# Kernel optimization log

Hardware: AMD Instinct MI355X
Metric: run time of the kernel (lower is better)

## Reference

```python
import jax, jax.numpy as jnp
import numpy as np

N = 100000      # num nodes (centers == sources here)
AVG_DEG = 16    # average degree -> ~1.6M edges
D_IN = 256
D_OUT = 128


def setup_inputs() -> dict:
    rng = np.random.default_rng(0)
    # random per-row degrees (some zeros allowed; gcn_norm masks inf -> 0)
    deg = rng.integers(0, 2 * AVG_DEG + 1, size=N)
    ptr = np.concatenate([[0], np.cumsum(deg)]).astype(np.int64)  # CSR row pointers [N+1]
    E = int(ptr[-1])
    idx = rng.integers(0, N, size=E).astype(np.int64)             # source node per edge
    dst = np.repeat(np.arange(N, dtype=np.int64), deg)            # destination node per edge

    key = jax.random.key(0)
    k1, k2 = jax.random.split(key)
    x = jax.random.normal(k1, (N, D_IN), dtype=jnp.float32)
    # glorot-ish init for Linear weight [out, in] (bias=False)
    W = jax.random.normal(k2, (D_OUT, D_IN), dtype=jnp.float32) * (1.0 / np.sqrt(D_IN))
    return {
        "x": x,
        "W": W,
        "ptr": jnp.asarray(ptr),
        "idx": jnp.asarray(idx),
        "dst": jnp.asarray(dst),
    }


def reference(x, W, ptr, idx, dst):
    # mm_before: in_channels (256) > out_channels (128) -> linear first
    h = x @ W.T  # [N, D_OUT]
    # gcn_norm: per-edge value = 1/deg(dst), inf -> 0
    deg = (ptr[1:] - ptr[:-1]).astype(jnp.float32)            # [N]
    inv_deg = jnp.where(deg > 0, 1.0 / jnp.maximum(deg, 1.0), 0.0)
    edge_value = inv_deg[dst]                                  # [E]
    # CSR weighted neighbor aggregation (SpMM): out[i] = sum_e ev[e] * h[idx[e]]
    msgs = h[idx] * edge_value[:, None]                        # [E, D_OUT]
    out = jax.ops.segment_sum(msgs, dst, num_segments=N)      # [N, D_OUT]
    return out
```

## Files before the change

### kernel.cpp

```cpp
#include <hip/hip_runtime.h>
#include <hip/hip_bf16.h>

typedef __attribute__((ext_vector_type(4))) float f32x4;
typedef __attribute__((ext_vector_type(8))) short s16x8;
typedef __attribute__((ext_vector_type(4))) short s16x4;
typedef __attribute__((ext_vector_type(4))) unsigned int u32x4;
typedef __attribute__((ext_vector_type(2))) unsigned int u32x2;

#define NODES 100000
#define SROW (NODES + 1)
#define DIN 256
#define DOUT 128
#define NSLICE 2
#define SLICE_CH 64

static __device__ inline unsigned short f2bf(float f) {
    __hip_bfloat16 h = __float2bfloat16(f);
    return __builtin_bit_cast(unsigned short, h);
}
static __device__ inline float lo2f(unsigned int v) {
    return __builtin_bit_cast(float, v << 16);
}
static __device__ inline float hi2f(unsigned int v) {
    return __builtin_bit_cast(float, v & 0xffff0000u);
}

__global__ __launch_bounds__(256) void gcn_prep(const float* __restrict__ W,
                                                const int* __restrict__ ptr,
                                                unsigned short* __restrict__ wsW,
                                                float* __restrict__ inv_deg,
                                                unsigned short* __restrict__ h_s) {
    int t = blockIdx.x * 256 + threadIdx.x;
    if (t < DOUT * DIN) wsW[t] = f2bf(W[t]);
    if (t < NODES) {
        int d = ptr[t + 1] - ptr[t];
        inv_deg[t] = d > 0 ? 1.0f / (float)d : 0.0f;
    }
    if (t < NSLICE * SLICE_CH)
        h_s[(long)(t >> 6) * ((long)SROW * SLICE_CH) + (long)NODES * SLICE_CH + (t & 63)] = 0;
}

__global__ __launch_bounds__(256) void gcn_gemm(const float* __restrict__ x,
                                                const unsigned short* __restrict__ wsW,
                                                unsigned short* __restrict__ h_s) {
    const int tid  = threadIdx.x;
    const int lane = tid & 63;
    const int wid  = tid >> 6;
    const int row0 = blockIdx.x * 128;
    const int lr = lane & 15;
    const int lg = lane >> 4;

    __shared__ unsigned short ldsA[128 * 64];
    __shared__ unsigned short ldsB[128 * 64];

    const int st_sub = tid >> 4;
    const int st_c4  = (tid & 15) * 4;

    f32x4 ar[8];
    u32x2 br[8];

#define LOADA(C) { _Pragma("unroll") for (int j = 0; j < 8; ++j) { \
        int grow = row0 + j * 16 + st_sub; \
        grow = grow < NODES ? grow : NODES - 1;  \
        ar[j] = *reinterpret_cast<const f32x4*>(x + (long)grow * DIN + (C) * 64 + st_c4); } }

#define LOADB(C) { _Pragma("unroll") for (int j = 0; j < 8; ++j) { \
        const int out = j * 16 + st_sub; \
        br[j] = *reinterpret_cast<const u32x2*>(wsW + out * DIN + (C) * 64 + st_c4); } }

#define STAGE() { _Pragma("unroll") for (int j = 0; j < 8; ++j) { \
        const int row = j * 16 + st_sub; \
        const int idx = row * 64 + (st_c4 ^ ((row & 7) << 3)); \
        s16x4 pa; \
        pa[0] = (short)f2bf(ar[j][0]); pa[1] = (short)f2bf(ar[j][1]); \
        pa[2] = (short)f2bf(ar[j][2]); pa[3] = (short)f2bf(ar[j][3]); \
        *reinterpret_cast<s16x4*>(ldsA + idx) = pa; \
        *reinterpret_cast<u32x2*>(ldsB + idx) = br[j]; } }

#define COMPUTE() { _Pragma("unroll") for (int ks = 0; ks < 2; ++ks) { \
        s16x8 a[2], b[8]; \
        _Pragma("unroll") for (int m = 0; m < 2; ++m) { \
            const int row = wid * 32 + m * 16 + lr; \
            const int idx = row * 64 + ((ks * 32 + lg * 8) ^ ((row & 7) << 3)); \
            a[m] = *reinterpret_cast<const s16x8*>(ldsA + idx); } \
        _Pragma("unroll") for (int n = 0; n < 8; ++n) { \
            const int out = n * 16 + lr; \
            const int idx = out * 64 + ((ks * 32 + lg * 8) ^ ((out & 7) << 3)); \
            b[n] = *reinterpret_cast<const s16x8*>(ldsB + idx); } \
        _Pragma("unroll") for (int n = 0; n < 8; ++n) { \
            acc[0][n] = __builtin_amdgcn_mfma_f32_16x16x32_bf16(a[0], b[n], acc[0][n], 0, 0, 0); \
            acc[1][n] = __builtin_amdgcn_mfma_f32_16x16x32_bf16(a[1], b[n], acc[1][n], 0, 0, 0); } } }

    f32x4 acc[2][8];
#pragma unroll
    for (int m = 0; m < 2; ++m)
#pragma unroll
        for (int n = 0; n < 8; ++n) acc[m][n] = (f32x4)(0.0f);

    LOADA(0); LOADB(0);
    STAGE();
    __syncthreads();
    LOADA(1); LOADB(1);
    COMPUTE();
    __syncthreads();
    STAGE();
    __syncthreads();
    LOADA(2); LOADB(2);
    COMPUTE();
    __syncthreads();
    STAGE();
    __syncthreads();
    LOADA(3); LOADB(3);
    COMPUTE();
    __syncthreads();
    STAGE();
    __syncthreads();
    COMPUTE();

#pragma unroll
    for (int m = 0; m < 2; ++m) {
        const int rbase = row0 + wid * 32 + m * 16 + lg * 4;
#pragma unroll
        for (int n = 0; n < 8; ++n) {
            const long sb = (long)(n >> 2) * ((long)SROW * SLICE_CH);
            const int ch = (n & 3) * 16 + lr;
#pragma unroll
            for (int r = 0; r < 4; ++r) {
                const int row = rbase + r;
                if (row < NODES)
                    h_s[sb + (long)row * SLICE_CH + ch] = f2bf(acc[m][n][r]);
            }
        }
    }
#undef LOADA
#undef LOADB
#undef STAGE
#undef COMPUTE
}

__global__ __launch_bounds__(320) void gcn_agg(const int* __restrict__ ptr,
                                               const int* __restrict__ idx,
                                               const unsigned short* __restrict__ h_s,
                                               const float* __restrict__ inv_deg,
                                               float* __restrict__ out, int E) {
    const int lane  = threadIdx.x & 63;
    const int wid   = threadIdx.x >> 6;
    const int q     = blockIdx.x & 7;
    const int slice = q >> 2;
    const int chunk = (blockIdx.x >> 3) * 4 + (q & 3);
    const int g     = lane >> 3;
    const int c     = lane & 7;
    const int node  = chunk * 40 + wid * 8 + g;

    const int p0  = ptr[node];
    const int deg = ptr[node + 1] - p0;
    const int Em1 = E - 1;
    const float w = inv_deg[node];

    int r[4];
#pragma unroll
    for (int j = 0; j < 4; ++j) {
        int a = p0 + c + 8 * j;
        a = a < Em1 ? a : Em1;
        r[j] = idx[a];
    }

    const unsigned short* hb = h_s + (long)slice * ((long)SROW * SLICE_CH) + c * 8;

    float acc[8];
#pragma unroll
    for (int t = 0; t < 8; ++t) acc[t] = 0.0f;

#pragma unroll
    for (int e = 0; e < 32; ++e) {
        int s = __shfl(r[e >> 3], (lane & 56) | (e & 7));
        s = e < deg ? s : NODES;
        const u32x4 v = *reinterpret_cast<const u32x4*>(hb + (long)s * SLICE_CH);
        acc[0] += lo2f(v[0]); acc[1] += hi2f(v[0]);
        acc[2] += lo2f(v[1]); acc[3] += hi2f(v[1]);
        acc[4] += lo2f(v[2]); acc[5] += hi2f(v[2]);
        acc[6] += lo2f(v[3]); acc[7] += hi2f(v[3]);
    }

    float* op = out + (long)node * DOUT + slice * SLICE_CH + c * 8;
    f32x4 o0, o1;
    o0[0] = acc[0] * w; o0[1] = acc[1] * w; o0[2] = acc[2] * w; o0[3] = acc[3] * w;
    o1[0] = acc[4] * w; o1[1] = acc[5] * w; o1[2] = acc[6] * w; o1[3] = acc[7] * w;
    *reinterpret_cast<f32x4*>(op) = o0;
    *reinterpret_cast<f32x4*>(op + 4) = o1;
}

extern "C" void kernel_launch(void* const* d_in, const int* in_sizes, int n_in,
                              void* d_out, int out_size, void* d_ws, size_t ws_size,
                              hipStream_t stream) {
    const float* x   = (const float*)d_in[0];
    const float* W   = (const float*)d_in[1];
    const int*   ptr = (const int*)d_in[2];
    const int*   idx = (const int*)d_in[3];
    float* out = (float*)d_out;
    const int E = in_sizes[3];

    char* ws = (char*)d_ws;
    unsigned short* wsW     = (unsigned short*)ws;
    float*          inv_deg = (float*)(ws + (64 << 10));
    unsigned short* h_s     = (unsigned short*)(ws + (1 << 20));

    gcn_prep<<<391, 256, 0, stream>>>(W, ptr, wsW, inv_deg, h_s);
    gcn_gemm<<<782, 256, 0, stream>>>(x, wsW, h_s);
    gcn_agg<<<5000, 320, 0, stream>>>(ptr, idx, h_s, inv_deg, out, E);
}
```

Before: 88.72 us.

## Double-buffer GEMM LDS tiles and stage epilogue through LDS for vector stores

The GEMM kernel now keeps two LDS buffers for the A/B tiles, so staging the next K-chunk overlaps with MFMA compute on the current one, which halves the number of barriers. The epilogue first writes bf16 results into a padded LDS tile and then emits 16-byte coalesced stores to the sliced h buffer, replacing scattered 2-byte stores. LDS use rises to 64KB per block, which may lower occupancy.

```diff
diff --git a/kernel.cpp b/kernel.cpp
--- a/kernel.cpp
+++ b/kernel.cpp
@@ -13,6 +13,7 @@
 #define DOUT 128
 #define NSLICE 2
 #define SLICE_CH 64
+#define EW 136
 
 static __device__ inline unsigned short f2bf(float f) {
     __hip_bfloat16 h = __float2bfloat16(f);
@@ -50,8 +51,12 @@
     const int lr = lane & 15;
     const int lg = lane >> 4;
 
-    __shared__ unsigned short ldsA[128 * 64];
-    __shared__ unsigned short ldsB[128 * 64];
+    __shared__ char smem[65536];
+    unsigned short* A0 = (unsigned short*)smem;
+    unsigned short* B0 = A0 + 8192;
+    unsigned short* A1 = B0 + 8192;
+    unsigned short* B1 = A1 + 8192;
+    unsigned short* EP = (unsigned short*)smem;
 
     const int st_sub = tid >> 4;
     const int st_c4  = (tid & 15) * 4;
@@ -68,25 +73,25 @@
         const int out = j * 16 + st_sub; \
         br[j] = *reinterpret_cast<const u32x2*>(wsW + out * DIN + (C) * 64 + st_c4); } }
 
-#define STAGE() { _Pragma("unroll") for (int j = 0; j < 8; ++j) { \
+#define STAGE(LA, LB) { _Pragma("unroll") for (int j = 0; j < 8; ++j) { \
         const int row = j * 16 + st_sub; \
         const int idx = row * 64 + (st_c4 ^ ((row & 7) << 3)); \
         s16x4 pa; \
         pa[0] = (short)f2bf(ar[j][0]); pa[1] = (short)f2bf(ar[j][1]); \
         pa[2] = (short)f2bf(ar[j][2]); pa[3] = (short)f2bf(ar[j][3]); \
-        *reinterpret_cast<s16x4*>(ldsA + idx) = pa; \
-        *reinterpret_cast<u32x2*>(ldsB + idx) = br[j]; } }
-
-#define COMPUTE() { _Pragma("unroll") for (int ks = 0; ks < 2; ++ks) { \
+        *reinterpret_cast<s16x4*>((LA) + idx) = pa; \
+        *reinterpret_cast<u32x2*>((LB) + idx) = br[j]; } }
+
+#define COMPUTE(LA, LB) { _Pragma("unroll") for (int ks = 0; ks < 2; ++ks) { \
         s16x8 a[2], b[8]; \
         _Pragma("unroll") for (int m = 0; m < 2; ++m) { \
             const int row = wid * 32 + m * 16 + lr; \
             const int idx = row * 64 + ((ks * 32 + lg * 8) ^ ((row & 7) << 3)); \
-            a[m] = *reinterpret_cast<const s16x8*>(ldsA + idx); } \
+            a[m] = *reinterpret_cast<const s16x8*>((LA) + idx); } \
         _Pragma("unroll") for (int n = 0; n < 8; ++n) { \
             const int out = n * 16 + lr; \
             const int idx = out * 64 + ((ks * 32 + lg * 8) ^ ((out & 7) << 3)); \
-            b[n] = *reinterpret_cast<const s16x8*>(ldsB + idx); } \
+            b[n] = *reinterpret_cast<const s16x8*>((LB) + idx); } \
         _Pragma("unroll") for (int n = 0; n < 8; ++n) { \
             acc[0][n] = __builtin_amdgcn_mfma_f32_16x16x32_bf16(a[0], b[n], acc[0][n], 0, 0, 0); \
             acc[1][n] = __builtin_amdgcn_mfma_f32_16x16x32_bf16(a[1], b[n], acc[1][n], 0, 0, 0); } } }
@@ -98,38 +103,44 @@
         for (int n = 0; n < 8; ++n) acc[m][n] = (f32x4)(0.0f);
 
     LOADA(0); LOADB(0);
-    STAGE();
-    __syncthreads();
+    STAGE(A0, B0);
     LOADA(1); LOADB(1);
-    COMPUTE();
-    __syncthreads();
-    STAGE();
-    __syncthreads();
+    __syncthreads();
+    STAGE(A1, B1);
     LOADA(2); LOADB(2);
-    COMPUTE();
-    __syncthreads();
-    STAGE();
-    __syncthreads();
+    COMPUTE(A0, B0);
+    __syncthreads();
+    STAGE(A0, B0);
     LOADA(3); LOADB(3);
-    COMPUTE();
-    __syncthreads();
-    STAGE();
-    __syncthreads();
-    COMPUTE();
+    COMPUTE(A1, B1);
+    __syncthreads();
+    STAGE(A1, B1);
+    COMPUTE(A0, B0);
+    __syncthreads();
+    COMPUTE(A1, B1);
+    __syncthreads();
 
 #pragma unroll
     for (int m = 0; m < 2; ++m) {
-        const int rbase = row0 + wid * 32 + m * 16 + lg * 4;
 #pragma unroll
         for (int n = 0; n < 8; ++n) {
-            const long sb = (long)(n >> 2) * ((long)SROW * SLICE_CH);
-            const int ch = (n & 3) * 16 + lr;
 #pragma unroll
             for (int r = 0; r < 4; ++r) {
-                const int row = rbase + r;
-                if (row < NODES)
-                    h_s[sb + (long)row * SLICE_CH + ch] = f2bf(acc[m][n][r]);
+                const int rl = wid * 32 + m * 16 + lg * 4 + r;
+                EP[rl * EW + n * 16 + lr] = f2bf(acc[m][n][r]);
             }
+        }
+    }
+    __syncthreads();
+#pragma unroll
+    for (int p = 0; p < 8; ++p) {
+        const int rl  = p * 16 + (tid >> 4);
+        const int ch0 = (tid & 15) * 8;
+        const int row = row0 + rl;
+        if (row < NODES) {
+            const s16x8 v = *reinterpret_cast<const s16x8*>(EP + rl * EW + ch0);
+            const long sb = (long)(ch0 >> 6) * ((long)SROW * SLICE_CH);
+            *reinterpret_cast<s16x8*>(h_s + sb + (long)row * SLICE_CH + (ch0 & 63)) = v;
         }
     }
 #undef LOADA
```

After: 88.08 us. About the same (-0.7%).
